# Optimization experiments

Measured on AMD Instinct MI355X. Metric: run time of the kernel, lower is better.

Reference implementation:

```python
import jax, jax.numpy as jnp
import numpy as np

B, N, C = 4, 100000, 64
S = 256            # img_size
RADIUS_PX = 1.5    # radius in pixels
K = 8              # points_per_pixel
GAMMA = 1.0
R_NDC = RADIUS_PX / S * 2.0  # radius in NDC, as in forward()


def setup_inputs() -> dict:
    key = jax.random.key(0)
    k1, k2 = jax.random.split(key)
    pts = jax.random.normal(k1, (B, N, 3), dtype=jnp.float32)
    features = jax.random.normal(k2, (B, N, C), dtype=jnp.float32)
    return {"pts": pts, "features": features}


def _rasterize_one(pts_b):
    # pts_b: (N,3) sign-flipped NDC points. Emulates pytorch3d rasterize_points:
    # per pixel keep the K nearest-in-z points whose NDC distance to the pixel
    # center is <= R_NDC (points with z < 0 are culled).
    x, y, z = pts_b[:, 0], pts_b[:, 1], pts_b[:, 2]
    # pytorch3d NDC->pixel: ndc = 1 - 2*(p+0.5)/S  =>  p = (1-ndc)*S/2 - 0.5
    px = (1.0 - x) * (S / 2.0) - 0.5
    py = (1.0 - y) * (S / 2.0) - 0.5
    offs = jnp.arange(-1, 3)  # 4-wide window fully covers a 1.5px radius
    cj = jnp.floor(px).astype(jnp.int32)[:, None] + offs  # (N,4) candidate cols
    ci = jnp.floor(py).astype(jnp.int32)[:, None] + offs  # (N,4) candidate rows
    cx = 1.0 - 2.0 * (cj.astype(pts_b.dtype) + 0.5) / S   # pixel-center NDC x
    cy = 1.0 - 2.0 * (ci.astype(pts_b.dtype) + 0.5) / S   # pixel-center NDC y
    d2 = (cy - y[:, None])[:, :, None] ** 2 + (cx - x[:, None])[:, None, :] ** 2  # (N,4,4)
    pid = ci[:, :, None] * S + cj[:, None, :]                                      # (N,4,4)
    inb = (ci[:, :, None] >= 0) & (ci[:, :, None] < S) & (cj[:, None, :] >= 0) & (cj[:, None, :] < S)
    valid = inb & (d2 <= R_NDC * R_NDC) & (z[:, None, None] >= 0.0)
    pid = jnp.where(valid, pid, S * S).reshape(-1)
    zc = jnp.where(valid, z[:, None, None], jnp.inf).reshape(-1)
    d2f = d2.reshape(-1)
    pidx = jnp.broadcast_to(jnp.arange(N, dtype=jnp.int32)[:, None, None], (N, 4, 4)).reshape(-1)
    order = jnp.lexsort((zc, pid))  # sort by pixel id, then depth (front first)
    pid_s, d2_s, pi_s = pid[order], d2f[order], pidx[order]
    seg_start = jnp.searchsorted(pid_s, pid_s, side='left')
    rank = jnp.arange(pid_s.shape[0]) - seg_start  # per-pixel z-rank
    keep = (pid_s < S * S) & (rank < K)
    pid_w = jnp.where(keep, pid_s, S * S)          # OOB index -> dropped by mode='drop'
    rank_w = jnp.where(keep, rank, 0)
    idx_buf = jnp.full((S * S, K), -1, jnp.int32).at[pid_w, rank_w].set(pi_s, mode='drop')
    d_buf = jnp.zeros((S * S, K), pts_b.dtype).at[pid_w, rank_w].set(d2_s, mode='drop')
    return idx_buf.reshape(S, S, K), d_buf.reshape(S, S, K)


def _forward(pts, features):
    # forward() flips x and y signs in-place
    pts = pts * jnp.array([-1.0, -1.0, 1.0], dtype=pts.dtype)
    idx, d2 = jax.vmap(_rasterize_one)(pts)        # (B,S,S,K) each
    dist = d2 / (R_NDC * R_NDC)
    alphas = 1.0 - jnp.clip(dist, 0.001, 1.0) ** (0.5 * GAMMA)  # .pow(0.5).pow(gamma)
    alphas = jnp.where(idx >= 0, alphas, 0.0)      # alpha_composite skips idx < 0
    trans = jnp.cumprod(1.0 - alphas, axis=-1)     # transmittance, front-to-back
    trans = jnp.concatenate([jnp.ones_like(trans[..., :1]), trans[..., :-1]], axis=-1)
    w = alphas * trans                             # (B,S,S,K) compositing weights
    gath = jax.vmap(lambda f, i: f[jnp.clip(i, 0)])(features, idx)  # (B,S,S,K,C)
    return jnp.einsum('bhwk,bhwkc->bchw', w, gath)  # (B,C,S,S)


def reference(pts, features):
    return _forward(pts, features)
```

## Files before the change

### kernel.cpp

```cpp
#include <hip/hip_runtime.h>
#include <stdint.h>

#pragma clang fp contract(off)

#define S 256
#define NPTS 100000
#define BATCH 4
#define CCH 64
#define K 8

static constexpr float R2 = 0.01171875f * 0.01171875f;
static constexpr unsigned long long SENT = 0xFFFFFFFFFFFFFFFFULL;

__global__ __launch_bounds__(256) void scatter_kernel(
        const float* __restrict__ pts,
        unsigned long long* __restrict__ keys) {
    int gid = blockIdx.x * blockDim.x + threadIdx.x;
    if (gid >= BATCH * NPTS * 16) return;
    int cell = gid & 15;
    int pid  = gid >> 4;
    int b = pid / NPTS;
    int n = pid - b * NPTS;

    const float* p = pts + (size_t)pid * 3;
    float x = -p[0];
    float y = -p[1];
    float z = p[2];
    if (!(z >= 0.0f)) return;

    float px = (1.0f - x) * 128.0f - 0.5f;
    float py = (1.0f - y) * 128.0f - 0.5f;
    int cj0 = (int)floorf(px);
    int ci0 = (int)floorf(py);

    int ci = ci0 - 1 + (cell >> 2);
    int cj = cj0 - 1 + (cell & 3);
    if (ci < 0 || ci >= S || cj < 0 || cj >= S) return;

    float cy = 1.0f - 2.0f * ((float)ci + 0.5f) / 256.0f;
    float cx = 1.0f - 2.0f * ((float)cj + 0.5f) / 256.0f;
    float dy = cy - y;
    float dx = cx - x;
    float d2 = dy * dy + dx * dx;
    if (!(d2 <= R2)) return;

    unsigned long long key =
        ((unsigned long long)__float_as_uint(z) << 32) | (unsigned int)n;
    unsigned long long* slot =
        keys + ((size_t)b * S * S + (size_t)(ci * S + cj)) * K;

    if (slot[K - 1] < key) return;

    for (int s = 0; s < K; ++s) {
        if (key == SENT) break;
        unsigned long long old = atomicMin(&slot[s], key);
        key = old > key ? old : key;
    }
}

__global__ __launch_bounds__(256) void blend_kernel(
        const float* __restrict__ pts,
        const float* __restrict__ feat,
        const unsigned long long* __restrict__ keys,
        float* __restrict__ out) {
    int seg = blockIdx.x;
    int h   = blockIdx.y;
    int b   = blockIdx.z;
    int tid = threadIdx.x;
    int w0  = seg * 64;

    __shared__ float s_alpha[64][K + 1];
    __shared__ float s_wgt[64][K + 1];
    __shared__ int   s_idx[64][K + 1];
    __shared__ int   s_cnt[64];

    const unsigned long long* kb =
        keys + ((size_t)b * S * S + (size_t)h * S + w0) * K;
    const float* pb = pts + (size_t)b * NPTS * 3;

    for (int e = tid; e < 64 * K; e += 256) {
        int p = e >> 3;
        int k = e & 7;
        unsigned long long key = kb[(size_t)p * K + k];
        float alpha = 0.0f;
        int idx = -1;
        if (key != SENT) {
            idx = (int)(unsigned int)(key & 0xFFFFFFFFULL);
            float x = -pb[(size_t)idx * 3 + 0];
            float y = -pb[(size_t)idx * 3 + 1];
            int w = w0 + p;
            float cy = 1.0f - 2.0f * ((float)h + 0.5f) / 256.0f;
            float cx = 1.0f - 2.0f * ((float)w + 0.5f) / 256.0f;
            float dy = cy - y;
            float dx = cx - x;
            float d2 = dy * dy + dx * dx;
            float dist = d2 / R2;
            dist = fminf(fmaxf(dist, 0.001f), 1.0f);
            alpha = 1.0f - sqrtf(dist);
        }
        s_alpha[p][k] = alpha;
        s_idx[p][k] = idx;
    }
    __syncthreads();

    if (tid < 64) {
        float t = 1.0f;
        int cnt = 0;
        for (int k = 0; k < K; ++k) {
            int raw = s_idx[tid][k];
            float a = s_alpha[tid][k];
            s_wgt[tid][k] = a * t;
            t *= (1.0f - a);
            if (raw >= 0) cnt = k + 1;
            s_idx[tid][k] = raw < 0 ? 0 : raw;
        }
        s_cnt[tid] = cnt;
    }
    __syncthreads();

    int wave = tid >> 6;
    int lane = tid & 63;
    int pbase = wave * 16;

    int kmax = 0;
#pragma unroll
    for (int i = 0; i < 16; ++i) {
        int c = s_cnt[pbase + i];
        kmax = c > kmax ? c : kmax;
    }

    float acc[16];
#pragma unroll
    for (int i = 0; i < 16; ++i) acc[i] = 0.0f;

    const float* fbl = feat + (size_t)b * NPTS * CCH + lane;
    for (int k = 0; k < kmax; ++k) {
        float v[16];
#pragma unroll
        for (int i = 0; i < 16; ++i) {
            int idx = s_idx[pbase + i][k];
            v[i] = fbl[(size_t)idx << 6];
        }
#pragma unroll
        for (int i = 0; i < 16; ++i) {
            acc[i] += s_wgt[pbase + i][k] * v[i];
        }
    }

    size_t obase = (((size_t)b * CCH + lane) * S + h) * S + (size_t)(w0 + pbase);
    float4* o4 = (float4*)(out + obase);
#pragma unroll
    for (int q = 0; q < 4; ++q) {
        o4[q] = make_float4(acc[4 * q + 0], acc[4 * q + 1],
                            acc[4 * q + 2], acc[4 * q + 3]);
    }
}

extern "C" void kernel_launch(void* const* d_in, const int* in_sizes, int n_in,
                              void* d_out, int out_size, void* d_ws, size_t ws_size,
                              hipStream_t stream) {
    const float* pts  = (const float*)d_in[0];
    const float* feat = (const float*)d_in[1];
    float* out = (float*)d_out;

    unsigned long long* keys = (unsigned long long*)d_ws;
    size_t key_bytes = (size_t)BATCH * S * S * K * sizeof(unsigned long long);
    hipMemsetAsync(keys, 0xFF, key_bytes, stream);

    int total = BATCH * NPTS * 16;
    scatter_kernel<<<(total + 255) / 256, 256, 0, stream>>>(pts, keys);

    dim3 grid(S / 64, S, BATCH);
    blend_kernel<<<grid, 256, 0, stream>>>(pts, feat, keys, out);
}
```

Measured before the change: 273.8 us.

## Replace atomicMin insertion with per-pixel append lists and separate top-K select

Scatter now appends each candidate key to a fixed-capacity per-pixel list via a single atomicAdd, and a new kernel sorts the first CAP entries per pixel to pick the K nearest in depth. This replaces chains of 64-bit atomicMin operations and the large sentinel memset with a small counts memset. It adds an extra kernel and more workspace traffic, and silently drops candidates if a pixel exceeds CAP entries; the old path is kept as a fallback when workspace is too small.

```diff
diff --git a/kernel.cpp b/kernel.cpp
--- a/kernel.cpp
+++ b/kernel.cpp
@@ -8,13 +8,15 @@
 #define BATCH 4
 #define CCH 64
 #define K 8
+#define CAP 20
 
 static constexpr float R2 = 0.01171875f * 0.01171875f;
 static constexpr unsigned long long SENT = 0xFFFFFFFFFFFFFFFFULL;
 
-__global__ __launch_bounds__(256) void scatter_kernel(
+__global__ __launch_bounds__(256) void scatter_list_kernel(
         const float* __restrict__ pts,
-        unsigned long long* __restrict__ keys) {
+        unsigned int* __restrict__ counts,
+        unsigned long long* __restrict__ lists) {
     int gid = blockIdx.x * blockDim.x + threadIdx.x;
     if (gid >= BATCH * NPTS * 16) return;
     int cell = gid & 15;
@@ -46,15 +48,52 @@
 
     unsigned long long key =
         ((unsigned long long)__float_as_uint(z) << 32) | (unsigned int)n;
-    unsigned long long* slot =
-        keys + ((size_t)b * S * S + (size_t)(ci * S + cj)) * K;
-
-    if (slot[K - 1] < key) return;
-
-    for (int s = 0; s < K; ++s) {
-        if (key == SENT) break;
-        unsigned long long old = atomicMin(&slot[s], key);
-        key = old > key ? old : key;
+    size_t base = (size_t)b * (S * S) + (size_t)(ci * S + cj);
+    unsigned int old = atomicAdd(&counts[base], 1u);
+    if (old < CAP) lists[base * CAP + old] = key;
+}
+
+__global__ __launch_bounds__(256) void select_topk_kernel(
+        const unsigned int* __restrict__ counts,
+        const unsigned long long* __restrict__ lists,
+        unsigned long long* __restrict__ keys) {
+    int pix = blockIdx.x * blockDim.x + threadIdx.x;
+    if (pix >= BATCH * S * S) return;
+
+    int c = (int)counts[pix];
+    if (c > CAP) c = CAP;
+    const ulonglong2* lp2 =
+        reinterpret_cast<const ulonglong2*>(lists + (size_t)pix * CAP);
+
+    unsigned long long v[CAP];
+#pragma unroll
+    for (int j = 0; j < CAP / 2; ++j) {
+        unsigned long long lo = SENT, hi = SENT;
+        if (2 * j < c) { ulonglong2 t = lp2[j]; lo = t.x; hi = t.y; }
+        v[2 * j] = lo;
+        v[2 * j + 1] = hi;
+    }
+#pragma unroll
+    for (int j = 0; j < CAP; ++j)
+        if (j >= c) v[j] = SENT;
+
+#pragma unroll
+    for (int i = 0; i < K; ++i) {
+#pragma unroll
+        for (int j = i + 1; j < CAP; ++j) {
+            unsigned long long a = v[i], q = v[j];
+            v[i] = a < q ? a : q;
+            v[j] = a < q ? q : a;
+        }
+    }
+
+    ulonglong2* kout = reinterpret_cast<ulonglong2*>(keys + (size_t)pix * K);
+#pragma unroll
+    for (int k = 0; k < K / 2; ++k) {
+        ulonglong2 t;
+        t.x = v[2 * k];
+        t.y = v[2 * k + 1];
+        kout[k] = t;
     }
 }
 
@@ -156,6 +195,52 @@
     }
 }
 
+__global__ __launch_bounds__(256) void scatter_kernel(
+        const float* __restrict__ pts,
+        unsigned long long* __restrict__ keys) {
+    int gid = blockIdx.x * blockDim.x + threadIdx.x;
+    if (gid >= BATCH * NPTS * 16) return;
+    int cell = gid & 15;
+    int pid  = gid >> 4;
+    int b = pid / NPTS;
+    int n = pid - b * NPTS;
+
+    const float* p = pts + (size_t)pid * 3;
+    float x = -p[0];
+    float y = -p[1];
+    float z = p[2];
+    if (!(z >= 0.0f)) return;
+
+    float px = (1.0f - x) * 128.0f - 0.5f;
+    float py = (1.0f - y) * 128.0f - 0.5f;
+    int cj0 = (int)floorf(px);
+    int ci0 = (int)floorf(py);
+
+    int ci = ci0 - 1 + (cell >> 2);
+    int cj = cj0 - 1 + (cell & 3);
+    if (ci < 0 || ci >= S || cj < 0 || cj >= S) return;
+
+    float cy = 1.0f - 2.0f * ((float)ci + 0.5f) / 256.0f;
+    float cx = 1.0f - 2.0f * ((float)cj + 0.5f) / 256.0f;
+    float dy = cy - y;
+    float dx = cx - x;
+    float d2 = dy * dy + dx * dx;
+    if (!(d2 <= R2)) return;
+
+    unsigned long long key =
+        ((unsigned long long)__float_as_uint(z) << 32) | (unsigned int)n;
+    unsigned long long* slot =
+        keys + ((size_t)b * S * S + (size_t)(ci * S + cj)) * K;
+
+    if (slot[K - 1] < key) return;
+
+    for (int s = 0; s < K; ++s) {
+        if (key == SENT) break;
+        unsigned long long old = atomicMin(&slot[s], key);
+        key = old > key ? old : key;
+    }
+}
+
 extern "C" void kernel_launch(void* const* d_in, const int* in_sizes, int n_in,
                               void* d_out, int out_size, void* d_ws, size_t ws_size,
                               hipStream_t stream) {
@@ -163,13 +248,36 @@
     const float* feat = (const float*)d_in[1];
     float* out = (float*)d_out;
 
-    unsigned long long* keys = (unsigned long long*)d_ws;
-    size_t key_bytes = (size_t)BATCH * S * S * K * sizeof(unsigned long long);
-    hipMemsetAsync(keys, 0xFF, key_bytes, stream);
-
-    int total = BATCH * NPTS * 16;
-    scatter_kernel<<<(total + 255) / 256, 256, 0, stream>>>(pts, keys);
-
-    dim3 grid(S / 64, S, BATCH);
-    blend_kernel<<<grid, 256, 0, stream>>>(pts, feat, keys, out);
-}
+    size_t cnt_bytes  = (size_t)BATCH * S * S * sizeof(unsigned int);
+    size_t list_bytes = (size_t)BATCH * S * S * CAP * sizeof(unsigned long long);
+    size_t key_bytes  = (size_t)BATCH * S * S * K * sizeof(unsigned long long);
+
+    if (ws_size >= cnt_bytes + list_bytes + key_bytes) {
+        unsigned int* counts = (unsigned int*)d_ws;
+        unsigned long long* lists =
+            (unsigned long long*)((char*)d_ws + cnt_bytes);
+        unsigned long long* dkeys =
+            (unsigned long long*)((char*)d_ws + cnt_bytes + list_bytes);
+        hipMemsetAsync(counts, 0, cnt_bytes, stream);
+
+        int total = BATCH * NPTS * 16;
+        scatter_list_kernel<<<(total + 255) / 256, 256, 0, stream>>>(
+            pts, counts, lists);
+
+        int npix = BATCH * S * S;
+        select_topk_kernel<<<(npix + 255) / 256, 256, 0, stream>>>(
+            counts, lists, dkeys);
+
+        dim3 grid(S / 64, S, BATCH);
+        blend_kernel<<<grid, 256, 0, stream>>>(pts, feat, dkeys, out);
+    } else {
+        unsigned long long* keys = (unsigned long long*)d_ws;
+        hipMemsetAsync(keys, 0xFF, key_bytes, stream);
+
+        int total = BATCH * NPTS * 16;
+        scatter_kernel<<<(total + 255) / 256, 256, 0, stream>>>(pts, keys);
+
+        dim3 grid(S / 64, S, BATCH);
+        blend_kernel<<<grid, 256, 0, stream>>>(pts, feat, keys, out);
+    }
+}
```

Result: faster. 261.1 us (-4.7%).
